# Performance work log

Measured on AMD Instinct MI355X. Metric: run time of the kernel, lower is better.

Reference implementation:

```python
import math
import jax, jax.numpy as jnp
import numpy as np

KS = 64        # top-k kept candidates per query
INIT_W = 16    # initial grid width
NEG = -1e9     # mask fill value


def setup_inputs() -> dict:
    key0 = jax.random.key(0)
    k1, k2, k3 = jax.random.split(key0, 3)
    N, T, H = 16, 2048, 64
    return {
        "query": jax.random.normal(k1, (N, T, H), jnp.float32),
        "key": jax.random.normal(k2, (N, T, H), jnp.float32),
        "value": jax.random.normal(k3, (N, T, H), jnp.float32),
    }


def _gather(x, idx):
    # x: [N, S, H], idx: [N, T, Z] -> [N, T, Z, H]
    return jnp.take_along_axis(x[:, None, :, :], idx[..., None], axis=2)


def _tree_indices(query, key):
    """Hierarchical tree top-k refinement (approx_mask): start from INIT_W
    coarse grid cells, repeatedly split each cell (scale_up=2), score the
    representative key of each cell against the query (sampled sparse matmul),
    and keep the top-KS cells, until cell width reaches 1 token."""
    N, T, H = query.shape
    S = key.shape[1]
    # causal per-row source length: tsrcs = arange(T_SRC+1-T_DST, T_SRC+1)
    tsrc = jnp.arange(S - T + 1, S + 1, dtype=jnp.float32)[None, :, None]  # [1,T,1]

    w = INIT_W
    zs = jnp.broadcast_to(jnp.arange(INIT_W, dtype=jnp.int32)[None, None, :], (N, T, INIT_W))
    mask = jnp.ones((N, T, INIT_W), dtype=bool)

    n_iter = int(math.log2(S // INIT_W))  # fixed iteration count (static shapes)
    for _ in range(n_iter):
        w2 = w * 2
        # resize: each cell z -> children (2z, 2z+1) on the finer grid
        zs = jnp.stack([zs * 2, zs * 2 + 1], axis=-1).reshape(N, T, -1)
        mask = jnp.repeat(mask, 2, axis=-1)
        # score representative key at cell start: pos = round(z * tsrc / w)
        pos = jnp.clip(jnp.round(zs.astype(jnp.float32) * (tsrc / w2)).astype(jnp.int32), 0, S - 1)
        scores = jnp.einsum('nth,ntzh->ntz', query, _gather(key, pos))
        scores = jnp.where(mask, scores, NEG)
        # topk_prime: keep top-k cells
        K = min(KS, zs.shape[-1])
        _, top_i = jax.lax.top_k(scores, K)
        zs = jnp.take_along_axis(zs, top_i, axis=-1)
        mask = jnp.take_along_axis(mask, top_i, axis=-1)
        w = w2
    # final token positions, causal validity
    pos = jnp.clip(jnp.round(zs.astype(jnp.float32) * (tsrc / w)).astype(jnp.int32), 0, S - 1)
    mask = mask & (pos.astype(jnp.float32) < tsrc)
    return pos, mask


def reference(query, key, value):
    N, T, H = query.shape
    pos, mask = _tree_indices(query, key)            # [N,T,K] int, bool
    ksel = _gather(key, pos)                          # [N,T,K,H]
    vsel = _gather(value, pos)                        # [N,T,K,H]
    scores = jnp.einsum('nth,ntzh->ntz', query, ksel) / math.sqrt(H)
    scores = jnp.where(mask, scores, NEG)
    p = jax.nn.softmax(scores, axis=-1)
    p = jnp.where(mask, p, 0.0)
    return jnp.einsum('ntz,ntzh->nth', p, vsel)
```

## Files before the change

kernel.cpp:

```cpp
#include <hip/hip_runtime.h>
#include <math.h>


constexpr int Tn = 2048;
constexpr int Hn = 64;
constexpr int WV = 4;
constexpr float NEGF = -1e9f;

__device__ __forceinline__ unsigned int ord32(float f) {
    unsigned int u = __float_as_uint(f);
    return (u & 0x80000000u) ? ~u : (u | 0x80000000u);
}

__device__ __forceinline__ unsigned long long packkey(float s, int e) {
    return ((unsigned long long)ord32(s) << 32) |
           (unsigned long long)(unsigned int)(~e);
}

__device__ __forceinline__ int cpos(int z, float ratio) {
    float x = (float)z * ratio;
    int p = (int)rintf(x);
    p = p < 0 ? 0 : p;
    p = p > (Tn - 1) ? (Tn - 1) : p;
    return p;
}

__device__ __forceinline__ float dotq(const float* __restrict__ krow,
                                      const float* qs) {
    float acc = 0.f;
#pragma unroll
    for (int h = 0; h < Hn; h += 4) {
        float4 kv = *reinterpret_cast<const float4*>(krow + h);
        float4 qv = *reinterpret_cast<const float4*>(qs + h);
        acc = fmaf(qv.x, kv.x, acc);
        acc = fmaf(qv.y, kv.y, acc);
        acc = fmaf(qv.z, kv.z, acc);
        acc = fmaf(qv.w, kv.w, acc);
    }
    return acc;
}

__global__ void TreeAttention_70257075028607_kernel(
        const float* __restrict__ Q, const float* __restrict__ Kk,
        const float* __restrict__ V, float* __restrict__ O) {
    __shared__ __align__(16) float              qsh[WV][Hn];
    __shared__ __align__(16) unsigned long long keysh[WV][128];
    __shared__ __align__(16) float              esch[WV][128];
    __shared__ __align__(16) int                ezh[WV][128];
    __shared__ __align__(16) float              nsch[WV][64];
    __shared__ __align__(16) int                nzh[WV][64];

    const int lane = threadIdx.x & 63;
    const int wv   = threadIdx.x >> 6;
    const int row  = blockIdx.x * WV + wv;
    const int n    = row >> 11;
    const int t    = row & (Tn - 1);
    const float tp1 = (float)(t + 1);

    const float* qrow = Q + (size_t)row * Hn;
    const float* Kb   = Kk + (size_t)n * Tn * Hn;
    const float* Vb   = V  + (size_t)n * Tn * Hn;

    float* qs = qsh[wv];
    unsigned long long* kz = keysh[wv];
    float* es = esch[wv];
    int*   ez = ezh[wv];
    float* ns = nsch[wv];
    int*   nz = nzh[wv];

    qs[lane] = qrow[lane];
    __syncthreads();

    int   myz  = 0;
    float mysc = NEGF;

    {
        const float ratio = tp1 * (1.0f / 32.0f);
        if (lane < 32) {
            float s = dotq(Kb + (size_t)cpos(lane, ratio) * Hn, qs);
            es[lane] = s;
            kz[lane] = packkey(s, lane);
        }
        __syncthreads();
        if (lane < 32) {
            unsigned long long mk = kz[lane];
            int r = 0;
#pragma unroll 8
            for (int j = 0; j < 32; ++j) r += (kz[j] > mk) ? 1 : 0;
            ns[r] = es[lane];
            nz[r] = lane;
        }
        __syncthreads();
        if (lane < 32) { myz = nz[lane]; mysc = ns[lane]; }
        __syncthreads();
    }

    {
        const float ratio = tp1 * (1.0f / 64.0f);
        if (lane < 32) {
            int z1 = 2 * myz + 1;
            float s1 = dotq(Kb + (size_t)cpos(z1, ratio) * Hn, qs);
            int e0 = 2 * lane;
            ez[e0]     = 2 * myz; es[e0]     = mysc; kz[e0]     = packkey(mysc, e0);
            ez[e0 + 1] = z1;      es[e0 + 1] = s1;   kz[e0 + 1] = packkey(s1, e0 + 1);
        }
        __syncthreads();
        {
            unsigned long long mk = kz[lane];
            int r = 0;
#pragma unroll 8
            for (int j = 0; j < 64; ++j) r += (kz[j] > mk) ? 1 : 0;
            ns[r] = es[lane];
            nz[r] = ez[lane];
        }
        __syncthreads();
        myz = nz[lane];
        mysc = ns[lane];
        __syncthreads();
    }

#pragma unroll
    for (int it = 0; it < 5; ++it) {
        const float ratio = tp1 * ldexpf(1.0f, -(7 + it));
        int z1 = 2 * myz + 1;
        float s1 = dotq(Kb + (size_t)cpos(z1, ratio) * Hn, qs);
        int e0 = 2 * lane;
        ez[e0]     = 2 * myz; es[e0]     = mysc; kz[e0]     = packkey(mysc, e0);
        ez[e0 + 1] = z1;      es[e0 + 1] = s1;   kz[e0 + 1] = packkey(s1, e0 + 1);
        __syncthreads();
        unsigned long long k0 = kz[lane];
        unsigned long long k1 = kz[lane + 64];
        int r0 = 0, r1 = 0;
        const ulonglong2* kp = reinterpret_cast<const ulonglong2*>(kz);
#pragma unroll 4
        for (int j = 0; j < 64; ++j) {
            ulonglong2 kj = kp[j];
            r0 += (kj.x > k0) ? 1 : 0;
            r0 += (kj.y > k0) ? 1 : 0;
            r1 += (kj.x > k1) ? 1 : 0;
            r1 += (kj.y > k1) ? 1 : 0;
        }
        if (r0 < 64) { ns[r0] = es[lane];      nz[r0] = ez[lane]; }
        if (r1 < 64) { ns[r1] = es[lane + 64]; nz[r1] = ez[lane + 64]; }
        __syncthreads();
        myz = nz[lane];
        mysc = ns[lane];
        __syncthreads();
    }

    {
        const float ratio = tp1 * (1.0f / 2048.0f);
        int  mypos = cpos(myz, ratio);
        bool valid = ((float)mypos < tp1);
        float s = valid ? mysc * 0.125f : NEGF;

        float m = s;
#pragma unroll
        for (int off = 32; off >= 1; off >>= 1)
            m = fmaxf(m, __shfl_xor(m, off, 64));
        float p = expf(s - m);
        float sum = p;
#pragma unroll
        for (int off = 32; off >= 1; off >>= 1)
            sum += __shfl_xor(sum, off, 64);
        p = p / sum;
        if (!valid) p = 0.f;

        ns[lane] = p;
        nz[lane] = mypos;
        __syncthreads();

        float acc = 0.f;
#pragma unroll 8
        for (int j = 0; j < 64; ++j) {
            acc = fmaf(ns[j], Vb[(size_t)nz[j] * Hn + lane], acc);
        }
        O[(size_t)row * Hn + lane] = acc;
    }
}

extern "C" void kernel_launch(void* const* d_in, const int* in_sizes, int n_in,
                              void* d_out, int out_size, void* d_ws, size_t ws_size,
                              hipStream_t stream) {
    const float* Q = (const float*)d_in[0];
    const float* K = (const float*)d_in[1];
    const float* V = (const float*)d_in[2];
    float* O = (float*)d_out;

    const int rows = in_sizes[0] / Hn;
    const int blocks = rows / WV;
    TreeAttention_70257075028607_kernel<<<blocks, WV * 64, 0, stream>>>(Q, K, V, O);
}
```

Measured before the change: 459.0 us.

## Replace rank-count top-k with bitonic sort and merge-path ranking, drop block barriers

Each refinement step used an O(n^2) rank count over 128 keys in shared memory. It now sorts the newly scored children with a wavefront-wide bitonic sort using shuffles. The already sorted kept parents are then merged with the new children by binary search ranking. Block-wide __syncthreads calls are replaced with an LDS waitcnt, on the assumption that each wavefront owns its own shared slice. Parent indices are recovered by shuffling from the source lane, which removes several shared arrays. This relies on wavefront lockstep execution to order LDS accesses within a wave, which is a correctness risk if the compiler reorders them.

Result: faster. 439.9 us (-4.2%).

```diff
diff --git a/kernel.cpp b/kernel.cpp
--- a/kernel.cpp
+++ b/kernel.cpp
@@ -7,15 +7,24 @@
 constexpr int WV = 4;
 constexpr float NEGF = -1e9f;
 
-__device__ __forceinline__ unsigned int ord32(float f) {
-    unsigned int u = __float_as_uint(f);
+typedef unsigned long long u64;
+typedef unsigned int u32;
+
+#define WWAIT() asm volatile("s_waitcnt lgkmcnt(0)" ::: "memory")
+
+__device__ __forceinline__ u32 ord32(float f) {
+    u32 u = __float_as_uint(f);
     return (u & 0x80000000u) ? ~u : (u | 0x80000000u);
 }
-
-__device__ __forceinline__ unsigned long long packkey(float s, int e) {
-    return ((unsigned long long)ord32(s) << 32) |
-           (unsigned long long)(unsigned int)(~e);
-}
+__device__ __forceinline__ u64 packkey(float s, int e) {
+    return ((u64)ord32(s) << 32) | (u64)(u32)(~e);
+}
+__device__ __forceinline__ float dec_score(u64 k) {
+    u32 o = (u32)(k >> 32);
+    u32 u = (o & 0x80000000u) ? (o & 0x7fffffffu) : ~o;
+    return __uint_as_float(u);
+}
+__device__ __forceinline__ int dec_e(u64 k) { return (int)(~(u32)k); }
 
 __device__ __forceinline__ int cpos(int z, float ratio) {
     float x = (float)z * ratio;
@@ -40,15 +49,44 @@
     return acc;
 }
 
-__global__ void TreeAttention_70257075028607_kernel(
+__device__ __forceinline__ u64 shflx64(u64 v, int m) {
+    u32 lo = (u32)__shfl_xor((int)(u32)v, m, 64);
+    u32 hi = (u32)__shfl_xor((int)(v >> 32), m, 64);
+    return ((u64)hi << 32) | lo;
+}
+
+template<int N>
+__device__ __forceinline__ u64 bitonic_desc(u64 key, int lane) {
+#pragma unroll
+    for (int k = 2; k <= N; k <<= 1) {
+#pragma unroll
+        for (int j = k >> 1; j >= 1; j >>= 1) {
+            u64 pk = shflx64(key, j);
+            bool wmax = (((lane & j) == 0) == ((lane & k) == 0));
+            key = ((key > pk) == wmax) ? key : pk;
+        }
+    }
+    return key;
+}
+
+template<int N>
+__device__ __forceinline__ int cnt_gt(const u64* D, u64 x) {
+    int c = 0;
+#pragma unroll
+    for (int s = N; s >= 1; s >>= 1) {
+        if (c + s <= N && D[c + s - 1] > x) c += s;
+    }
+    return c;
+}
+
+__global__ void __launch_bounds__(256)
+TreeAttention_70257075028607_kernel(
         const float* __restrict__ Q, const float* __restrict__ Kk,
         const float* __restrict__ V, float* __restrict__ O) {
-    __shared__ __align__(16) float              qsh[WV][Hn];
-    __shared__ __align__(16) unsigned long long keysh[WV][128];
-    __shared__ __align__(16) float              esch[WV][128];
-    __shared__ __align__(16) int                ezh[WV][128];
-    __shared__ __align__(16) float              nsch[WV][64];
-    __shared__ __align__(16) int                nzh[WV][64];
+    __shared__ __align__(16) float qsh[WV][Hn];
+    __shared__ __align__(16) u64   Lsh[WV][64];
+    __shared__ __align__(16) u64   Rsh[WV][64];
+    __shared__ __align__(16) u64   Osh[WV][64];
 
     const int lane = threadIdx.x & 63;
     const int wv   = threadIdx.x >> 6;
@@ -62,95 +100,79 @@
     const float* Vb   = V  + (size_t)n * Tn * Hn;
 
     float* qs = qsh[wv];
-    unsigned long long* kz = keysh[wv];
-    float* es = esch[wv];
-    int*   ez = ezh[wv];
-    float* ns = nsch[wv];
-    int*   nz = nzh[wv];
+    u64* Lb = Lsh[wv];
+    u64* Rb = Rsh[wv];
+    u64* Ob = Osh[wv];
 
     qs[lane] = qrow[lane];
-    __syncthreads();
+    WWAIT();
 
     int   myz  = 0;
     float mysc = NEGF;
 
     {
-        const float ratio = tp1 * (1.0f / 32.0f);
+        const float ratio = tp1 * (1.f / 32.f);
+        u64 key;
         if (lane < 32) {
             float s = dotq(Kb + (size_t)cpos(lane, ratio) * Hn, qs);
-            es[lane] = s;
-            kz[lane] = packkey(s, lane);
-        }
-        __syncthreads();
+            key = packkey(s, lane);
+        } else {
+            key = (u64)lane;
+        }
+        key = bitonic_desc<32>(key, lane);
+        if (lane < 32) { myz = dec_e(key); mysc = dec_score(key); }
+    }
+
+    {
+        const float ratio = tp1 * (1.f / 64.f);
+        u64 Lk = packkey(mysc, 2 * lane);
+        u64 Rs;
         if (lane < 32) {
-            unsigned long long mk = kz[lane];
-            int r = 0;
-#pragma unroll 8
-            for (int j = 0; j < 32; ++j) r += (kz[j] > mk) ? 1 : 0;
-            ns[r] = es[lane];
-            nz[r] = lane;
-        }
-        __syncthreads();
-        if (lane < 32) { myz = nz[lane]; mysc = ns[lane]; }
-        __syncthreads();
-    }
-
-    {
-        const float ratio = tp1 * (1.0f / 64.0f);
+            float s1 = dotq(Kb + (size_t)cpos(2 * myz + 1, ratio) * Hn, qs);
+            Rs = packkey(s1, 2 * lane + 1);
+        } else {
+            Rs = (u64)lane;
+        }
+        Rs = bitonic_desc<32>(Rs, lane);
+        if (lane < 32) { Lb[lane] = Lk; Rb[lane] = Rs; }
+        WWAIT();
         if (lane < 32) {
-            int z1 = 2 * myz + 1;
-            float s1 = dotq(Kb + (size_t)cpos(z1, ratio) * Hn, qs);
-            int e0 = 2 * lane;
-            ez[e0]     = 2 * myz; es[e0]     = mysc; kz[e0]     = packkey(mysc, e0);
-            ez[e0 + 1] = z1;      es[e0 + 1] = s1;   kz[e0 + 1] = packkey(s1, e0 + 1);
-        }
-        __syncthreads();
-        {
-            unsigned long long mk = kz[lane];
-            int r = 0;
-#pragma unroll 8
-            for (int j = 0; j < 64; ++j) r += (kz[j] > mk) ? 1 : 0;
-            ns[r] = es[lane];
-            nz[r] = ez[lane];
-        }
-        __syncthreads();
-        myz = nz[lane];
-        mysc = ns[lane];
-        __syncthreads();
+            int rL = lane + cnt_gt<32>(Rb, Lk);
+            int rR = lane + cnt_gt<32>(Lb, Rs);
+            Ob[rL] = Lk;
+            Ob[rR] = Rs;
+        }
+        WWAIT();
+        u64 kk = Ob[lane];
+        int e  = dec_e(kk);
+        int pz = __shfl(myz, e >> 1, 64);
+        myz  = 2 * pz + (e & 1);
+        mysc = dec_score(kk);
     }
 
 #pragma unroll
     for (int it = 0; it < 5; ++it) {
         const float ratio = tp1 * ldexpf(1.0f, -(7 + it));
-        int z1 = 2 * myz + 1;
-        float s1 = dotq(Kb + (size_t)cpos(z1, ratio) * Hn, qs);
-        int e0 = 2 * lane;
-        ez[e0]     = 2 * myz; es[e0]     = mysc; kz[e0]     = packkey(mysc, e0);
-        ez[e0 + 1] = z1;      es[e0 + 1] = s1;   kz[e0 + 1] = packkey(s1, e0 + 1);
-        __syncthreads();
-        unsigned long long k0 = kz[lane];
-        unsigned long long k1 = kz[lane + 64];
-        int r0 = 0, r1 = 0;
-        const ulonglong2* kp = reinterpret_cast<const ulonglong2*>(kz);
-#pragma unroll 4
-        for (int j = 0; j < 64; ++j) {
-            ulonglong2 kj = kp[j];
-            r0 += (kj.x > k0) ? 1 : 0;
-            r0 += (kj.y > k0) ? 1 : 0;
-            r1 += (kj.x > k1) ? 1 : 0;
-            r1 += (kj.y > k1) ? 1 : 0;
-        }
-        if (r0 < 64) { ns[r0] = es[lane];      nz[r0] = ez[lane]; }
-        if (r1 < 64) { ns[r1] = es[lane + 64]; nz[r1] = ez[lane + 64]; }
-        __syncthreads();
-        myz = nz[lane];
-        mysc = ns[lane];
-        __syncthreads();
+        float s1 = dotq(Kb + (size_t)cpos(2 * myz + 1, ratio) * Hn, qs);
+        u64 Lk = packkey(mysc, 2 * lane);
+        u64 Rs = bitonic_desc<64>(packkey(s1, 2 * lane + 1), lane);
+        Lb[lane] = Lk;
+        Rb[lane] = Rs;
+        WWAIT();
+        int rL = lane + cnt_gt<64>(Rb, Lk);
+        int rR = lane + cnt_gt<64>(Lb, Rs);
+        if (rL < 64) Ob[rL] = Lk;
+        if (rR < 64) Ob[rR] = Rs;
+        WWAIT();
+        u64 kk = Ob[lane];
+        int e  = dec_e(kk);
+        int pz = __shfl(myz, e >> 1, 64);
+        myz  = 2 * pz + (e & 1);
+        mysc = dec_score(kk);
     }
 
     {
-        const float ratio = tp1 * (1.0f / 2048.0f);
-        int  mypos = cpos(myz, ratio);
+        int mypos  = cpos(myz, tp1 * (1.f / 2048.f));
         bool valid = ((float)mypos < tp1);
         float s = valid ? mysc * 0.125f : NEGF;
 
@@ -166,14 +188,15 @@
         p = p / sum;
         if (!valid) p = 0.f;
 
-        ns[lane] = p;
-        nz[lane] = mypos;
-        __syncthreads();
+        Ob[lane] = ((u64)(u32)mypos << 32) | __float_as_uint(p);
+        WWAIT();
 
         float acc = 0.f;
 #pragma unroll 8
-        for (int j = 0; j < 64; ++j) {
-            acc = fmaf(ns[j], Vb[(size_t)nz[j] * Hn + lane], acc);
+        for (int jj = 0; jj < 64; ++jj) {
+            u64 w = Ob[jj];
+            acc = fmaf(__uint_as_float((u32)w),
+                       Vb[(size_t)(w >> 32) * Hn + lane], acc);
         }
         O[(size_t)row * Hn + lane] = acc;
     }
```
